# Optimization experiments

Hardware: AMD Instinct MI355X
Metric: run time of the kernel (lower is better)

Reference implementation:

```python
import jax, jax.numpy as jnp
import numpy as np

F = 256  # features
B, N = 16, 2048


def setup_inputs() -> dict:
    key = jax.random.key(0)
    ks = jax.random.split(key, 12)
    s = 1.0 / np.sqrt(F)
    return {
        "x": jax.random.normal(ks[0], (B, N, F), dtype=jnp.float32),
        "p": jax.random.normal(ks[1], (B, N, 3), dtype=jnp.float32),
        # nn.Linear weights: [out, in], y = x @ W.T + b
        "Wq": jax.random.normal(ks[2], (F, F), dtype=jnp.float32) * s,
        "bq": jax.random.normal(ks[3], (F,), dtype=jnp.float32) * s,
        "Wk": jax.random.normal(ks[4], (F, F), dtype=jnp.float32) * s,
        "bk": jax.random.normal(ks[5], (F,), dtype=jnp.float32) * s,
        "Wv": jax.random.normal(ks[6], (F, F), dtype=jnp.float32) * s,
        "bv": jax.random.normal(ks[7], (F,), dtype=jnp.float32) * s,
        # Conv1d kernel_size=1 == pointwise linear: W1 [F,3], W2 [F,F]
        "W1": jax.random.normal(ks[8], (F, 3), dtype=jnp.float32) * (1.0 / np.sqrt(3.0)),
        "b1": jax.random.normal(ks[9], (F,), dtype=jnp.float32) * (1.0 / np.sqrt(3.0)),
        "W2": jax.random.normal(ks[10], (F, F), dtype=jnp.float32) * s,
        "b2": jax.random.normal(ks[11], (F,), dtype=jnp.float32) * s,
    }


def reference(x, p, Wq, bq, Wk, bk, Wv, bv, W1, b1, W2, b2):
    # Positional encoder: Conv1d(3->F, k=1) + ReLU + Conv1d(F->F, k=1)
    pos = jnp.maximum(p @ W1.T + b1, 0.0) @ W2.T + b2  # [B, N, F]
    h = x + pos
    # NOTE: the original code swaps names: x_query = self.key(x), x_key = self.query(x)
    q = h @ Wk.T + bk  # x_query
    k = h @ Wq.T + bq  # x_key
    v = h @ Wv.T + bv  # x_value
    scale = 1.0 / np.sqrt(float(F))
    scores = jnp.einsum("bnf,bmf->bnm", q, k) * scale  # [B, N, N]
    attn = jax.nn.softmax(scores, axis=-1)
    return jnp.einsum("bnm,bmf->bnf", attn, v)  # [B, N, F]
```

## Files before the change

kernel.cpp:

```cpp
#include <hip/hip_runtime.h>

#define FEAT 256
#define SEQ  2048
#define NBATCH 16

typedef float  f32x4  __attribute__((ext_vector_type(4)));
typedef __bf16 bf16x8 __attribute__((ext_vector_type(8)));

__device__ __forceinline__ unsigned short f2bf(float f) {
  union { float f; unsigned int u; } v; v.f = f;
  unsigned int r = (v.u + 0x7fffu + ((v.u >> 16) & 1u)) >> 16;
  return (unsigned short)r;
}
__device__ __forceinline__ float bf2f(unsigned short u) {
  union { unsigned int u; float f; } v; v.u = ((unsigned int)u) << 16;
  return v.f;
}
__device__ __forceinline__ unsigned int pack2bf(float a, float b) {
  return (unsigned int)f2bf(a) | ((unsigned int)f2bf(b) << 16);
}

__device__ __forceinline__ float redsum16(float t) {
  t += __shfl_xor(t, 1);
  t += __shfl_xor(t, 2);
  t += __shfl_xor(t, 4);
  t += __shfl_xor(t, 8);
  return t;
}

__device__ __forceinline__ void gld16(const unsigned short* g, unsigned short* l) {
  __builtin_amdgcn_global_load_lds(
      (const __attribute__((address_space(1))) unsigned int*)(const void*)g,
      (__attribute__((address_space(3))) unsigned int*)(void*)l, 16, 0, 0);
}

__global__ __launch_bounds__(256) void k_wcvt(
    const float* __restrict__ Wq, const float* __restrict__ Wk,
    const float* __restrict__ Wv, const float* __restrict__ W2,
    unsigned short* __restrict__ Wqb, unsigned short* __restrict__ Wkb,
    unsigned short* __restrict__ Wvb, unsigned short* __restrict__ W2b) {
  int i = blockIdx.x * 256 + threadIdx.x;
  Wqb[i] = f2bf(Wq[i]);
  Wkb[i] = f2bf(Wk[i]);
  Wvb[i] = f2bf(Wv[i]);
  W2b[i] = f2bf(W2[i]);
}

__global__ __launch_bounds__(256) void k_pos_h(
    const float* __restrict__ x, const float* __restrict__ p,
    const float* __restrict__ W1, const float* __restrict__ b1,
    const unsigned short* __restrict__ W2b, const float* __restrict__ b2,
    unsigned short* __restrict__ hb) {
  __shared__ __align__(16) unsigned short tlds[64 * 264];
  __shared__ float pl[192];
  const int tid = threadIdx.x;
  const int blk = blockIdx.x;
  const int tok0 = blk * 64;
  if (tid < 192) pl[tid] = p[tok0 * 3 + tid];
  __syncthreads();
  const int j = tid;
  const float w0 = W1[j * 3 + 0], w1 = W1[j * 3 + 1], w2 = W1[j * 3 + 2];
  const float bb = b1[j];
#pragma unroll 4
  for (int tl = 0; tl < 64; ++tl) {
    float v = bb + pl[tl * 3 + 0] * w0 + pl[tl * 3 + 1] * w1 + pl[tl * 3 + 2] * w2;
    v = v > 0.f ? v : 0.f;
    tlds[tl * 264 + j] = f2bf(v);
  }
  __syncthreads();
  const int w = tid >> 6, lane = tid & 63;
  const int col = lane & 15, quad = lane >> 4;
  bf16x8 af[8];
  const unsigned short* arow = tlds + (w * 16 + col) * 264 + quad * 8;
#pragma unroll
  for (int ks = 0; ks < 8; ++ks) af[ks] = *(const bf16x8*)(arow + ks * 32);
#pragma unroll 1
  for (int ct = 0; ct < 16; ++ct) {
    f32x4 acc = {0.f, 0.f, 0.f, 0.f};
    const unsigned short* brow = W2b + (ct * 16 + col) * 256 + quad * 8;
#pragma unroll
    for (int ks = 0; ks < 8; ++ks) {
      bf16x8 bf = *(const bf16x8*)(brow + ks * 32);
      acc = __builtin_amdgcn_mfma_f32_16x16x32_bf16(af[ks], bf, acc, 0, 0, 0);
    }
    const int f = ct * 16 + col;
    const float bias = b2[f];
#pragma unroll
    for (int r = 0; r < 4; ++r) {
      const int tok = tok0 + w * 16 + quad * 4 + r;
      float v = acc[r] + bias + x[tok * 256 + f];
      hb[tok * 256 + f] = f2bf(v);
    }
  }
}

__global__ __launch_bounds__(256) void k_qkv(
    const unsigned short* __restrict__ hb,
    const unsigned short* __restrict__ Wqb, const float* __restrict__ bq,
    const unsigned short* __restrict__ Wkb, const float* __restrict__ bk,
    const unsigned short* __restrict__ Wvb, const float* __restrict__ bv,
    unsigned short* __restrict__ qb, unsigned short* __restrict__ kb,
    unsigned short* __restrict__ vtb) {
  const int tid = threadIdx.x, blk = blockIdx.x;
  const int ct0 = blockIdx.y * 8;
  const int w = tid >> 6, lane = tid & 63;
  const int col = lane & 15, quad = lane >> 4;
  const int row0 = blk * 128 + w * 32;
  bf16x8 af0[8], af1[8];
  const unsigned short* arow0 = hb + (size_t)(row0 + col) * 256 + quad * 8;
  const unsigned short* arow1 = arow0 + 16 * 256;
#pragma unroll
  for (int ks = 0; ks < 8; ++ks) {
    af0[ks] = *(const bf16x8*)(arow0 + ks * 32);
    af1[ks] = *(const bf16x8*)(arow1 + ks * 32);
  }
#pragma unroll 1
  for (int mat = 0; mat < 3; ++mat) {
    const unsigned short* W = (mat == 0) ? Wkb : ((mat == 1) ? Wqb : Wvb);
    const float* bias = (mat == 0) ? bk : ((mat == 1) ? bq : bv);
#pragma unroll 1
    for (int ct = ct0; ct < ct0 + 8; ++ct) {
      f32x4 a0 = {0.f, 0.f, 0.f, 0.f}, a1 = {0.f, 0.f, 0.f, 0.f};
      const unsigned short* brow = W + (ct * 16 + col) * 256 + quad * 8;
#pragma unroll
      for (int ks = 0; ks < 8; ++ks) {
        bf16x8 bf = *(const bf16x8*)(brow + ks * 32);
        a0 = __builtin_amdgcn_mfma_f32_16x16x32_bf16(af0[ks], bf, a0, 0, 0, 0);
        a1 = __builtin_amdgcn_mfma_f32_16x16x32_bf16(af1[ks], bf, a1, 0, 0, 0);
      }
      const int f = ct * 16 + col;
      const float bs = bias[f];
      if (mat == 0) {
#pragma unroll
        for (int r = 0; r < 4; ++r) {
          qb[(size_t)(row0 + quad * 4 + r) * 256 + f] = f2bf(a0[r] + bs);
          qb[(size_t)(row0 + 16 + quad * 4 + r) * 256 + f] = f2bf(a1[r] + bs);
        }
      } else if (mat == 1) {
        const int ks_ = f >> 5, qk = (f >> 3) & 3, jj = f & 7;
#pragma unroll
        for (int r = 0; r < 4; ++r) {
          const int tok = row0 + quad * 4 + r;
          const int b0 = tok >> 11, n = tok & 2047;
          const int g = n >> 5, key = n & 31;
          const size_t base =
              ((((size_t)(b0 * 64 + g) * 8 + ks_) * 4 + qk) * 32);
          kb[(base + key) * 8 + jj] = f2bf(a0[r] + bs);
          kb[(base + key + 16) * 8 + jj] = f2bf(a1[r] + bs);
        }
      } else {
        uint4 pk;
        pk.x = pack2bf(a0[0] + bs, a1[0] + bs);
        pk.y = pack2bf(a0[1] + bs, a1[1] + bs);
        pk.z = pack2bf(a0[2] + bs, a1[2] + bs);
        pk.w = pack2bf(a0[3] + bs, a1[3] + bs);
        const int t0 = row0 + quad * 4;
        const int b0 = t0 >> 11, n = t0 & 2047;
        const int g = n >> 5;
        *(uint4*)(vtb + (((size_t)(b0 * 64 + g) * 4 + quad) * 256 + f) * 8) = pk;
      }
    }
  }
}

__global__ __launch_bounds__(256, 2) void k_attn(
    const unsigned short* __restrict__ qb, const unsigned short* __restrict__ kb,
    const unsigned short* __restrict__ vtb, float* __restrict__ outA,
    unsigned short* __restrict__ obB, float* __restrict__ lbuf) {
  __shared__ __align__(16) unsigned short Kl[2][8192];
  __shared__ __align__(16) unsigned short Vt[2][8192];
  __shared__ __align__(16) unsigned short Pl[4][32 * 40];
  const int tid = threadIdx.x;
  const int bx = blockIdx.x, b = blockIdx.y, h = blockIdx.z;
  const int w = tid >> 6, lane = tid & 63;
  const int col = lane & 15, quad = lane >> 4;
  const int n0 = bx * 128 + w * 32;
  const float scale = 0.0625f;

  bf16x8 qf0[8], qf1[8];
  const unsigned short* qrow0 = qb + (size_t)(b * 2048 + n0 + col) * 256 + quad * 8;
  const unsigned short* qrow1 = qrow0 + 16 * 256;
#pragma unroll
  for (int ks = 0; ks < 8; ++ks) {
    qf0[ks] = *(const bf16x8*)(qrow0 + ks * 32);
    qf1[ks] = *(const bf16x8*)(qrow1 + ks * 32);
  }

  f32x4 O0[16], O1[16];
#pragma unroll
  for (int ft = 0; ft < 16; ++ft) {
    O0[ft] = (f32x4){0.f, 0.f, 0.f, 0.f};
    O1[ft] = (f32x4){0.f, 0.f, 0.f, 0.f};
  }
  float ls0[4], ls1[4];
#pragma unroll
  for (int r = 0; r < 4; ++r) { ls0[r] = 0.f; ls1[r] = 0.f; }

  const unsigned short* kbase = kb + (size_t)b * 64 * 8192;
  const unsigned short* vbase = vtb + (size_t)b * 64 * 8192;
  unsigned short* Pw = Pl[w];
  const int kt0 = h * 32;
  const int sl = w * 2048 + lane * 8;

#pragma unroll
  for (int q = 0; q < 4; ++q) {
    gld16(kbase + (size_t)kt0 * 8192 + sl + q * 512, &Kl[0][sl + q * 512]);
    gld16(vbase + (size_t)kt0 * 8192 + sl + q * 512, &Vt[0][sl + q * 512]);
  }

  for (int kt2 = 0; kt2 < 32; ++kt2) {
    const int cur = kt2 & 1;
    const unsigned short* Kc = Kl[cur];
    const unsigned short* Vc = Vt[cur];
    __syncthreads();
    if (kt2 + 1 < 32) {
      const size_t tb = (size_t)(kt0 + kt2 + 1) * 8192;
#pragma unroll
      for (int q = 0; q < 4; ++q) {
        gld16(kbase + tb + sl + q * 512, &Kl[cur ^ 1][sl + q * 512]);
        gld16(vbase + tb + sl + q * 512, &Vt[cur ^ 1][sl + q * 512]);
      }
    }
    f32x4 s00 = {0.f, 0.f, 0.f, 0.f}, s01 = {0.f, 0.f, 0.f, 0.f};
    f32x4 s10 = {0.f, 0.f, 0.f, 0.f}, s11 = {0.f, 0.f, 0.f, 0.f};
#pragma unroll
    for (int ks = 0; ks < 8; ++ks) {
      const unsigned short* kc = Kc + (ks * 4 + quad) * 256 + col * 8;
      bf16x8 k0 = *(const bf16x8*)(kc);
      bf16x8 k1 = *(const bf16x8*)(kc + 128);
      s00 = __builtin_amdgcn_mfma_f32_16x16x32_bf16(qf0[ks], k0, s00, 0, 0, 0);
      s01 = __builtin_amdgcn_mfma_f32_16x16x32_bf16(qf0[ks], k1, s01, 0, 0, 0);
      s10 = __builtin_amdgcn_mfma_f32_16x16x32_bf16(qf1[ks], k0, s10, 0, 0, 0);
      s11 = __builtin_amdgcn_mfma_f32_16x16x32_bf16(qf1[ks], k1, s11, 0, 0, 0);
    }
#pragma unroll
    for (int r = 0; r < 4; ++r) {
      float p0 = __expf(fmaf(s00[r], scale, -8.0f));
      float p1 = __expf(fmaf(s01[r], scale, -8.0f));
      ls0[r] += p0 + p1;
      *(unsigned int*)(Pw + (quad * 4 + r) * 40 + 2 * col) = pack2bf(p0, p1);
      float q0 = __expf(fmaf(s10[r], scale, -8.0f));
      float q1 = __expf(fmaf(s11[r], scale, -8.0f));
      ls1[r] += q0 + q1;
      *(unsigned int*)(Pw + (16 + quad * 4 + r) * 40 + 2 * col) = pack2bf(q0, q1);
    }
    bf16x8 pf0 = *(const bf16x8*)(Pw + col * 40 + quad * 8);
    bf16x8 pf1 = *(const bf16x8*)(Pw + (16 + col) * 40 + quad * 8);
#pragma unroll
    for (int ft = 0; ft < 16; ++ft) {
      bf16x8 vf = *(const bf16x8*)(Vc + quad * 2048 + (ft * 16 + col) * 8);
      O0[ft] = __builtin_amdgcn_mfma_f32_16x16x32_bf16(pf0, vf, O0[ft], 0, 0, 0);
      O1[ft] = __builtin_amdgcn_mfma_f32_16x16x32_bf16(pf1, vf, O1[ft], 0, 0, 0);
    }
  }
  float sr0[4], sr1[4];
#pragma unroll
  for (int r = 0; r < 4; ++r) {
    sr0[r] = redsum16(ls0[r]);
    sr1[r] = redsum16(ls1[r]);
  }
  if (h == 0) {
    if (col == 0) {
#pragma unroll
      for (int r = 0; r < 4; ++r) {
        lbuf[b * 2048 + n0 + quad * 4 + r] = sr0[r];
        lbuf[b * 2048 + n0 + 16 + quad * 4 + r] = sr1[r];
      }
    }
#pragma unroll
    for (int ft = 0; ft < 16; ++ft) {
#pragma unroll
      for (int r = 0; r < 4; ++r) {
        const int n = n0 + quad * 4 + r;
        outA[(size_t)(b * 2048 + n) * 256 + ft * 16 + col] = O0[ft][r];
        outA[(size_t)(b * 2048 + n + 16) * 256 + ft * 16 + col] = O1[ft][r];
      }
    }
  } else {
    if (col == 0) {
#pragma unroll
      for (int r = 0; r < 4; ++r) {
        lbuf[32768 + b * 2048 + n0 + quad * 4 + r] = sr0[r];
        lbuf[32768 + b * 2048 + n0 + 16 + quad * 4 + r] = sr1[r];
      }
    }
#pragma unroll
    for (int ft = 0; ft < 16; ++ft) {
#pragma unroll
      for (int r = 0; r < 4; ++r) {
        const int n = n0 + quad * 4 + r;
        obB[(size_t)(b * 2048 + n) * 256 + ft * 16 + col] = f2bf(O0[ft][r]);
        obB[(size_t)(b * 2048 + n + 16) * 256 + ft * 16 + col] = f2bf(O1[ft][r]);
      }
    }
  }
}

__global__ __launch_bounds__(256) void k_reduce(
    float* __restrict__ out, const unsigned short* __restrict__ ob,
    const float* __restrict__ lbuf) {
  const size_t i4 = (size_t)blockIdx.x * 256 + threadIdx.x;
  const int bn = (int)(i4 >> 6);
  const float rl = 1.0f / (lbuf[bn] + lbuf[32768 + bn]);
  float4 o = ((const float4*)out)[i4];
  ushort4 b4 = ((const ushort4*)ob)[i4];
  o.x = (o.x + bf2f(b4.x)) * rl;
  o.y = (o.y + bf2f(b4.y)) * rl;
  o.z = (o.z + bf2f(b4.z)) * rl;
  o.w = (o.w + bf2f(b4.w)) * rl;
  ((float4*)out)[i4] = o;
}

extern "C" void kernel_launch(void* const* d_in, const int* in_sizes, int n_in,
                              void* d_out, int out_size, void* d_ws, size_t ws_size,
                              hipStream_t stream) {
  const float* x  = (const float*)d_in[0];
  const float* p  = (const float*)d_in[1];
  const float* Wq = (const float*)d_in[2];
  const float* bq = (const float*)d_in[3];
  const float* Wk = (const float*)d_in[4];
  const float* bk = (const float*)d_in[5];
  const float* Wv = (const float*)d_in[6];
  const float* bv = (const float*)d_in[7];
  const float* W1 = (const float*)d_in[8];
  const float* b1 = (const float*)d_in[9];
  const float* W2 = (const float*)d_in[10];
  const float* b2 = (const float*)d_in[11];
  float* out = (float*)d_out;

  char* ws = (char*)d_ws;
  unsigned short* W2b = (unsigned short*)(ws + 0);
  unsigned short* Wqb = (unsigned short*)(ws + 131072);
  unsigned short* Wkb = (unsigned short*)(ws + 262144);
  unsigned short* Wvb = (unsigned short*)(ws + 393216);
  unsigned short* hb  = (unsigned short*)(ws + 524288);
  unsigned short* qb  = (unsigned short*)(ws + 524288 + 16777216);
  unsigned short* kb  = (unsigned short*)(ws + 524288 + 2 * 16777216);
  unsigned short* vtb = (unsigned short*)(ws + 524288 + 3 * 16777216);
  float* lbuf = (float*)(ws + 524288 + 4 * 16777216);

  k_wcvt<<<256, 256, 0, stream>>>(Wq, Wk, Wv, W2, Wqb, Wkb, Wvb, W2b);
  k_pos_h<<<512, 256, 0, stream>>>(x, p, W1, b1, W2b, b2, hb);
  k_qkv<<<dim3(256, 2), 256, 0, stream>>>(hb, Wqb, bq, Wkb, bk, Wvb, bv, qb, kb, vtb);
  k_attn<<<dim3(16, 16, 2), 256, 0, stream>>>(qb, kb, vtb, out, hb, lbuf);
  k_reduce<<<8192, 256, 0, stream>>>(out, hb, lbuf);
}
```

Baseline: 279.2 us.

## Fuse positional encoder into QKV projection and use exp2 in softmax

Merges the pos-encoder/h kernel with the QKV projection kernel so h stays in shared memory per 64-token tile instead of round-tripping through global memory, which also removes one launch. Each block now does all three projections for its 64 tokens, with four waves split across row halves and column halves. The attention exponent now uses exp2f with pre-scaled log2e constants instead of __expf. The tradeoff is fewer blocks working on QKV (512 with 64 rows each versus 512 with 128 rows over 2 column halves), which may change occupancy and how much weight data gets reused.

```diff
diff --git a/kernel.cpp b/kernel.cpp
--- a/kernel.cpp
+++ b/kernel.cpp
@@ -46,73 +46,71 @@
   W2b[i] = f2bf(W2[i]);
 }
 
-__global__ __launch_bounds__(256) void k_pos_h(
+__global__ __launch_bounds__(256) void k_posqkv(
     const float* __restrict__ x, const float* __restrict__ p,
     const float* __restrict__ W1, const float* __restrict__ b1,
     const unsigned short* __restrict__ W2b, const float* __restrict__ b2,
-    unsigned short* __restrict__ hb) {
-  __shared__ __align__(16) unsigned short tlds[64 * 264];
-  __shared__ float pl[192];
-  const int tid = threadIdx.x;
-  const int blk = blockIdx.x;
-  const int tok0 = blk * 64;
-  if (tid < 192) pl[tid] = p[tok0 * 3 + tid];
-  __syncthreads();
-  const int j = tid;
-  const float w0 = W1[j * 3 + 0], w1 = W1[j * 3 + 1], w2 = W1[j * 3 + 2];
-  const float bb = b1[j];
-#pragma unroll 4
-  for (int tl = 0; tl < 64; ++tl) {
-    float v = bb + pl[tl * 3 + 0] * w0 + pl[tl * 3 + 1] * w1 + pl[tl * 3 + 2] * w2;
-    v = v > 0.f ? v : 0.f;
-    tlds[tl * 264 + j] = f2bf(v);
-  }
-  __syncthreads();
-  const int w = tid >> 6, lane = tid & 63;
-  const int col = lane & 15, quad = lane >> 4;
-  bf16x8 af[8];
-  const unsigned short* arow = tlds + (w * 16 + col) * 264 + quad * 8;
-#pragma unroll
-  for (int ks = 0; ks < 8; ++ks) af[ks] = *(const bf16x8*)(arow + ks * 32);
-#pragma unroll 1
-  for (int ct = 0; ct < 16; ++ct) {
-    f32x4 acc = {0.f, 0.f, 0.f, 0.f};
-    const unsigned short* brow = W2b + (ct * 16 + col) * 256 + quad * 8;
-#pragma unroll
-    for (int ks = 0; ks < 8; ++ks) {
-      bf16x8 bf = *(const bf16x8*)(brow + ks * 32);
-      acc = __builtin_amdgcn_mfma_f32_16x16x32_bf16(af[ks], bf, acc, 0, 0, 0);
-    }
-    const int f = ct * 16 + col;
-    const float bias = b2[f];
-#pragma unroll
-    for (int r = 0; r < 4; ++r) {
-      const int tok = tok0 + w * 16 + quad * 4 + r;
-      float v = acc[r] + bias + x[tok * 256 + f];
-      hb[tok * 256 + f] = f2bf(v);
-    }
-  }
-}
-
-__global__ __launch_bounds__(256) void k_qkv(
-    const unsigned short* __restrict__ hb,
     const unsigned short* __restrict__ Wqb, const float* __restrict__ bq,
     const unsigned short* __restrict__ Wkb, const float* __restrict__ bk,
     const unsigned short* __restrict__ Wvb, const float* __restrict__ bv,
     unsigned short* __restrict__ qb, unsigned short* __restrict__ kb,
     unsigned short* __restrict__ vtb) {
+  __shared__ __align__(16) unsigned short tlds[64 * 264];
+  __shared__ float pl[192];
   const int tid = threadIdx.x, blk = blockIdx.x;
-  const int ct0 = blockIdx.y * 8;
+  const int tok0 = blk * 64;
+  if (tid < 192) pl[tid] = p[tok0 * 3 + tid];
+  __syncthreads();
+  {
+    const int j = tid;
+    const float w0 = W1[j * 3 + 0], w1 = W1[j * 3 + 1], w2 = W1[j * 3 + 2];
+    const float bb = b1[j];
+#pragma unroll 4
+    for (int tl = 0; tl < 64; ++tl) {
+      float v = bb + pl[tl * 3 + 0] * w0 + pl[tl * 3 + 1] * w1 + pl[tl * 3 + 2] * w2;
+      v = v > 0.f ? v : 0.f;
+      tlds[tl * 264 + j] = f2bf(v);
+    }
+  }
+  __syncthreads();
   const int w = tid >> 6, lane = tid & 63;
   const int col = lane & 15, quad = lane >> 4;
-  const int row0 = blk * 128 + w * 32;
+  {
+    bf16x8 af[8];
+    const unsigned short* arow = tlds + (w * 16 + col) * 264 + quad * 8;
+#pragma unroll
+    for (int ks = 0; ks < 8; ++ks) af[ks] = *(const bf16x8*)(arow + ks * 32);
+    __syncthreads();
+#pragma unroll 1
+    for (int ct = 0; ct < 16; ++ct) {
+      f32x4 acc = {0.f, 0.f, 0.f, 0.f};
+      const unsigned short* brow = W2b + (ct * 16 + col) * 256 + quad * 8;
+#pragma unroll
+      for (int ks = 0; ks < 8; ++ks) {
+        bf16x8 bf = *(const bf16x8*)(brow + ks * 32);
+        acc = __builtin_amdgcn_mfma_f32_16x16x32_bf16(af[ks], bf, acc, 0, 0, 0);
+      }
+      const int f = ct * 16 + col;
+      const float bias = b2[f];
+#pragma unroll
+      for (int r = 0; r < 4; ++r) {
+        const int tl = w * 16 + quad * 4 + r;
+        float v = acc[r] + bias + x[(size_t)(tok0 + tl) * 256 + f];
+        tlds[tl * 264 + f] = f2bf(v);
+      }
+    }
+  }
+  __syncthreads();
+  const int row0l = (w >> 1) * 32;
+  const int row0 = tok0 + row0l;
+  const int ct0 = (w & 1) * 8;
   bf16x8 af0[8], af1[8];
-  const unsigned short* arow0 = hb + (size_t)(row0 + col) * 256 + quad * 8;
-  const unsigned short* arow1 = arow0 + 16 * 256;
+  const unsigned short* a0r = tlds + (row0l + col) * 264 + quad * 8;
+  const unsigned short* a1r = a0r + 16 * 264;
 #pragma unroll
   for (int ks = 0; ks < 8; ++ks) {
-    af0[ks] = *(const bf16x8*)(arow0 + ks * 32);
-    af1[ks] = *(const bf16x8*)(arow1 + ks * 32);
+    af0[ks] = *(const bf16x8*)(a0r + ks * 32);
+    af1[ks] = *(const bf16x8*)(a1r + ks * 32);
   }
 #pragma unroll 1
   for (int mat = 0; mat < 3; ++mat) {
@@ -175,7 +173,8 @@
   const int w = tid >> 6, lane = tid & 63;
   const int col = lane & 15, quad = lane >> 4;
   const int n0 = bx * 128 + w * 32;
-  const float scale = 0.0625f;
+  const float sc2 = 0.09016844f;
+  const float bo2 = -11.5415603f;
 
   bf16x8 qf0[8], qf1[8];
   const unsigned short* qrow0 = qb + (size_t)(b * 2048 + n0 + col) * 256 + quad * 8;
@@ -235,12 +234,12 @@
     }
 #pragma unroll
     for (int r = 0; r < 4; ++r) {
-      float p0 = __expf(fmaf(s00[r], scale, -8.0f));
-      float p1 = __expf(fmaf(s01[r], scale, -8.0f));
+      float p0 = exp2f(fmaf(s00[r], sc2, bo2));
+      float p1 = exp2f(fmaf(s01[r], sc2, bo2));
       ls0[r] += p0 + p1;
       *(unsigned int*)(Pw + (quad * 4 + r) * 40 + 2 * col) = pack2bf(p0, p1);
-      float q0 = __expf(fmaf(s10[r], scale, -8.0f));
-      float q1 = __expf(fmaf(s11[r], scale, -8.0f));
+      float q0 = exp2f(fmaf(s10[r], sc2, bo2));
+      float q1 = exp2f(fmaf(s11[r], sc2, bo2));
       ls1[r] += q0 + q1;
       *(unsigned int*)(Pw + (16 + quad * 4 + r) * 40 + 2 * col) = pack2bf(q0, q1);
     }
@@ -333,15 +332,15 @@
   unsigned short* Wqb = (unsigned short*)(ws + 131072);
   unsigned short* Wkb = (unsigned short*)(ws + 262144);
   unsigned short* Wvb = (unsigned short*)(ws + 393216);
-  unsigned short* hb  = (unsigned short*)(ws + 524288);
+  unsigned short* obB = (unsigned short*)(ws + 524288);
   unsigned short* qb  = (unsigned short*)(ws + 524288 + 16777216);
   unsigned short* kb  = (unsigned short*)(ws + 524288 + 2 * 16777216);
   unsigned short* vtb = (unsigned short*)(ws + 524288 + 3 * 16777216);
   float* lbuf = (float*)(ws + 524288 + 4 * 16777216);
 
   k_wcvt<<<256, 256, 0, stream>>>(Wq, Wk, Wv, W2, Wqb, Wkb, Wvb, W2b);
-  k_pos_h<<<512, 256, 0, stream>>>(x, p, W1, b1, W2b, b2, hb);
-  k_qkv<<<dim3(256, 2), 256, 0, stream>>>(hb, Wqb, bq, Wkb, bk, Wvb, bv, qb, kb, vtb);
-  k_attn<<<dim3(16, 16, 2), 256, 0, stream>>>(qb, kb, vtb, out, hb, lbuf);
-  k_reduce<<<8192, 256, 0, stream>>>(out, hb, lbuf);
-}
+  k_posqkv<<<512, 256, 0, stream>>>(x, p, W1, b1, W2b, b2,
+                                    Wqb, bq, Wkb, bk, Wvb, bv, qb, kb, vtb);
+  k_attn<<<dim3(16, 16, 2), 256, 0, stream>>>(qb, kb, vtb, out, obB, lbuf);
+  k_reduce<<<8192, 256, 0, stream>>>(out, obB, lbuf);
+}
```

New measurement: 279.1 us. No clear change (-0.0%).
